# Optimization experiments

Measured on AMD Instinct MI355X. Metric: run time of the kernel, lower is better.

## Reference

```python
import jax, jax.numpy as jnp
import numpy as np

N_HEADS = 6
HEAD_SIZE = 64


def setup_inputs() -> dict:
    key = jax.random.key(0)
    k1, k2, k3, k4 = jax.random.split(key, 4)
    B, T, C = 8, 2048, N_HEADS * HEAD_SIZE
    x = jax.random.normal(k1, (B, T, C), dtype=jnp.float32)
    # small init scale keeps softmax logits in a sane range
    w_qkv = jax.random.normal(k2, (C, 3 * C), dtype=jnp.float32) * 0.05
    w_proj = jax.random.normal(k3, (C, C), dtype=jnp.float32) * 0.05
    b_proj = jax.random.normal(k4, (C,), dtype=jnp.float32) * 0.05
    return {"x": x, "w_qkv": w_qkv, "w_proj": w_proj, "b_proj": b_proj}


def reference(x, w_qkv, w_proj, b_proj):
    B, T, C = x.shape
    qkv = x @ w_qkv                      # [B, T, 3C]
    q, k, v = jnp.split(qkv, 3, axis=2)
    # [B, T, C] -> [B, H, T, D]
    def heads(t):
        return t.reshape(B, T, N_HEADS, HEAD_SIZE).transpose(0, 2, 1, 3)
    q, k, v = heads(q), heads(k), heads(v)
    scale = HEAD_SIZE ** -0.5
    scores = jnp.einsum('bhqd,bhkd->bhqk', q, k) * scale   # [B, H, T, T]
    causal = jnp.tril(jnp.ones((T, T), dtype=bool))
    scores = jnp.where(causal[None, None], scores, jnp.float32(-jnp.inf))
    weights = jax.nn.softmax(scores, axis=-1)
    # dropout is identity in eval mode
    out = jnp.einsum('bhqk,bhkd->bhqd', weights, v)          # [B, H, T, D]
    out = out.transpose(0, 2, 1, 3).reshape(B, T, C)
    return out @ w_proj + b_proj
```

## Files before the change

kernel.cpp:

```cpp
#include <hip/hip_runtime.h>
#include <hip/hip_bf16.h>

typedef __bf16 bf16_t;
typedef __bf16 bf16x8 __attribute__((ext_vector_type(8)));
typedef __bf16 bf16x4 __attribute__((ext_vector_type(4)));
typedef float floatx4 __attribute__((ext_vector_type(4)));
typedef unsigned uint32x2 __attribute__((ext_vector_type(2)));

#define MFMA16(a, b, c) __builtin_amdgcn_mfma_f32_16x16x32_bf16(a, b, c, 0, 0, 0)

#if __has_builtin(__builtin_amdgcn_exp2f)
#define EXP2F(x) __builtin_amdgcn_exp2f(x)
#else
#define EXP2F(x) __expf((x)*0.693147180559945f)
#endif

__device__ __forceinline__ void async_copy16(const bf16_t* g, bf16_t* l) {
    __builtin_amdgcn_global_load_lds((const __attribute__((address_space(1))) void*)g,
                                     (__attribute__((address_space(3))) void*)l, 16, 0, 0);
}

__device__ __forceinline__ unsigned cvt_pk_bf16(float lo, float hi) {
    unsigned r;
    asm("v_cvt_pk_bf16_f32 %0, %1, %2" : "=v"(r) : "v"(lo), "v"(hi));
    return r;
}

__device__ __forceinline__ void plane32(unsigned& x, unsigned& y) {
#if __has_builtin(__builtin_amdgcn_permlane32_swap)
    uint32x2 r = __builtin_amdgcn_permlane32_swap(x, y, false, false);
    x = r[0]; y = r[1];
#else
    asm("v_permlane32_swap_b32 %0, %1" : "+v"(x), "+v"(y));
#endif
}
__device__ __forceinline__ void plane16(unsigned& x, unsigned& y) {
#if __has_builtin(__builtin_amdgcn_permlane16_swap)
    uint32x2 r = __builtin_amdgcn_permlane16_swap(x, y, false, false);
    x = r[0]; y = r[1];
#else
    asm("v_permlane16_swap_b32 %0, %1" : "+v"(x), "+v"(y));
#endif
}

__device__ __forceinline__ bf16x8 pack_pfrag(const floatx4& sE, const floatx4& sO) {
    unsigned a0 = cvt_pk_bf16(sE[0], sE[1]);
    unsigned a1 = cvt_pk_bf16(sE[2], sE[3]);
    unsigned b0 = cvt_pk_bf16(sO[0], sO[1]);
    unsigned b1 = cvt_pk_bf16(sO[2], sO[3]);
    plane32(a0, b0);
    plane32(a1, b1);
    plane16(a0, b0);
    plane16(a1, b1);
    union { unsigned u[4]; bf16x8 v; } r;
    r.u[0] = a0; r.u[1] = a1; r.u[2] = b0; r.u[3] = b1;
    return r.v;
}

__global__ void prep_fused(const float* __restrict__ w_qkv, const float* __restrict__ w_proj,
                           bf16_t* __restrict__ wqkvT, bf16_t* __restrict__ wprojT) {
    const int bx = blockIdx.x, tid = threadIdx.x;
    __shared__ float tile[32][33];
    int which, n0, k0, Nd;
    if (bx < 432) {
        which = 0; Nd = 1152; n0 = (bx % 36) * 32; k0 = (bx / 36) * 32;
    } else {
        int idx = bx - 432;
        which = 1; Nd = 384; n0 = (idx % 12) * 32; k0 = (idx / 12) * 32;
    }
    const float* in = which ? w_proj : w_qkv;
    bf16_t* out = which ? wprojT : wqkvT;
    const int tx = tid & 31, ty = tid >> 5;
#pragma unroll
    for (int i = 0; i < 4; i++)
        tile[ty + i * 8][tx] = in[(size_t)(k0 + ty + i * 8) * Nd + n0 + tx];
    __syncthreads();
#pragma unroll
    for (int i = 0; i < 4; i++) {
        int n = n0 + ty + i * 8;
        float v = tile[tx][ty + i * 8];
        if (!which && n < 384) v *= 0.1803368851f;
        out[(size_t)n * 384 + k0 + tx] = (bf16_t)v;
    }
}

__global__ __launch_bounds__(256, 3)
void gemm_qkv(const float* __restrict__ X, const bf16_t* __restrict__ Bt,
              bf16_t* __restrict__ qkv, bf16_t* __restrict__ Vt, int M, int N, int K) {
    __shared__ __align__(16) bf16_t As[2][128 * 32];
    __shared__ __align__(16) bf16_t Bs[2][128 * 32];
    const int nblk = blockIdx.x;
    const int wgl = ((nblk & 7) * 144) + (nblk >> 3);
    const int row0 = (wgl / 9) * 128, col0 = (wgl % 9) * 128;
    const int tid = threadIdx.x;
    const int wave = tid >> 6, lane = tid & 63;
    const int wm = wave >> 1, wn = wave & 1;
    const int quad = lane >> 4, l16 = lane & 15;
    const int swz = l16 & 3;

    floatx4 acc[4][4];
#pragma unroll
    for (int i = 0; i < 4; i++)
#pragma unroll
        for (int j = 0; j < 4; j++) acc[i][j] = (floatx4){0.f, 0.f, 0.f, 0.f};

    float4 stg[4];
    auto a_load = [&](int k0) {
#pragma unroll
        for (int it = 0; it < 2; it++) {
            int c = wave * 64 + it * 256 + lane;
            int r = c >> 2;
            int col = k0 + (((c & 3) ^ (r & 3)) * 8);
            const float* src = X + (size_t)(row0 + r) * K + col;
            stg[it * 2 + 0] = *(const float4*)src;
            stg[it * 2 + 1] = *(const float4*)(src + 4);
        }
    };
    auto a_write = [&](int buf) {
#pragma unroll
        for (int it = 0; it < 2; it++) {
            float4 v0 = stg[it * 2 + 0], v1 = stg[it * 2 + 1];
            bf16x8 o = {(bf16_t)v0.x, (bf16_t)v0.y, (bf16_t)v0.z, (bf16_t)v0.w,
                        (bf16_t)v1.x, (bf16_t)v1.y, (bf16_t)v1.z, (bf16_t)v1.w};
            *(bf16x8*)(&As[buf][0] + (size_t)(wave * 64 + it * 256 + lane) * 8) = o;
        }
    };
    auto b_stage = [&](int buf, int k0) {
#pragma unroll
        for (int it = 0; it < 2; it++) {
            int cb = wave * 64 + it * 256;
            int c = cb + lane;
            int r = c >> 2;
            int col = k0 + (((c & 3) ^ (r & 3)) * 8);
            async_copy16(Bt + (size_t)(col0 + r) * K + col, &Bs[buf][0] + cb * 8);
        }
    };

    const int nk = K >> 5;
    a_load(0);
    b_stage(0, 0);
    a_write(0);
    for (int kt = 0; kt < nk; kt++) {
        __syncthreads();
        const bool more = (kt + 1 < nk);
        if (more) {
            a_load((kt + 1) * 32);
            b_stage((kt + 1) & 1, (kt + 1) * 32);
        }
        const bf16_t* as = &As[kt & 1][0];
        const bf16_t* bs = &Bs[kt & 1][0];
        bf16x8 af[4], bfr[4];
#pragma unroll
        for (int i = 0; i < 4; i++)
            af[i] = *(const bf16x8*)(as + (wm * 64 + i * 16 + l16) * 32 + ((quad ^ swz) * 8));
#pragma unroll
        for (int j = 0; j < 4; j++)
            bfr[j] = *(const bf16x8*)(bs + (wn * 64 + j * 16 + l16) * 32 + ((quad ^ swz) * 8));
#pragma unroll
        for (int i = 0; i < 4; i++)
#pragma unroll
            for (int j = 0; j < 4; j++) acc[i][j] = MFMA16(bfr[j], af[i], acc[i][j]);
        if (more) a_write((kt + 1) & 1);
    }
    if (col0 < 768) {
#pragma unroll
        for (int i = 0; i < 4; i++) {
            const size_t row = (size_t)(row0 + wm * 64 + i * 16 + l16);
#pragma unroll
            for (int j = 0; j < 4; j++) {
                const int colb = col0 + wn * 64 + j * 16 + quad * 4;
                bf16x4 v = {(bf16_t)acc[i][j][0], (bf16_t)acc[i][j][1],
                            (bf16_t)acc[i][j][2], (bf16_t)acc[i][j][3]};
                *(bf16x4*)(qkv + row * N + colb) = v;
            }
        }
    } else {
        __syncthreads();
        bf16_t* myb = &As[0][0] + wave * 4096;
#pragma unroll
        for (int i = 0; i < 4; i++)
#pragma unroll
            for (int j = 0; j < 4; j++)
#pragma unroll
                for (int r = 0; r < 4; r++) {
                    int d2 = j * 16 + quad * 4 + r;
                    int t2 = i * 16 + l16;
                    myb[d2 * 64 + (((t2 >> 3) ^ (d2 & 7)) * 8) + (t2 & 7)] =
                        (bf16_t)acc[i][j][r];
                }
        asm volatile("s_waitcnt lgkmcnt(0)" ::: "memory");
        const int row_t = row0 + wm * 64;
        const int b = row_t >> 11;
        const int tt = (row_t & 2047) >> 6;
        const int h = (col0 - 768 + wn * 64) >> 6;
        bf16_t* vout = Vt + (((size_t)(b * 6 + h) * 32 + tt) << 12);
#pragma unroll
        for (int it = 0; it < 8; it++) {
            int d2 = it * 8 + (lane >> 3);
            int cl = lane & 7;
            bf16x8 v = *(const bf16x8*)(myb + d2 * 64 + ((cl ^ (d2 & 7)) * 8));
            *(bf16x8*)(vout + d2 * 64 + cl * 8) = v;
        }
    }
}

__global__ __launch_bounds__(256, 3)
void gemm_out(const bf16_t* __restrict__ A, const bf16_t* __restrict__ Bt,
              float* __restrict__ C, int M, int N, int K, const float* __restrict__ bias) {
    __shared__ __align__(16) bf16_t As[2][64 * 32];
    __shared__ __align__(16) bf16_t Bs[2][128 * 32];
    const int nblk = blockIdx.x;
    const int wgl = ((nblk & 7) * 96) + (nblk >> 3);
    const int row0 = (wgl / 3) * 64, col0 = (wgl % 3) * 128;
    const int tid = threadIdx.x;
    const int wave = tid >> 6, lane = tid & 63;
    const int wm = wave >> 1, wn = wave & 1;
    const int quad = lane >> 4, l16 = lane & 15;
    const int swz = l16 & 3;

    floatx4 acc[2][4];
#pragma unroll
    for (int i = 0; i < 2; i++)
#pragma unroll
        for (int j = 0; j < 4; j++) acc[i][j] = (floatx4){0.f, 0.f, 0.f, 0.f};

    auto stage = [&](int buf, int k0) {
        {
            int c = wave * 64 + lane;
            int r = c >> 2;
            int col = k0 + (((c & 3) ^ (r & 3)) * 8);
            async_copy16(A + (size_t)(row0 + r) * K + col, &As[buf][0] + (wave * 64) * 8);
        }
#pragma unroll
        for (int it = 0; it < 2; it++) {
            int cb = wave * 64 + it * 256;
            int c = cb + lane;
            int r = c >> 2;
            int col = k0 + (((c & 3) ^ (r & 3)) * 8);
            async_copy16(Bt + (size_t)(col0 + r) * K + col, &Bs[buf][0] + cb * 8);
        }
    };

    const int nk = K >> 5;
    stage(0, 0);
    for (int kt = 0; kt < nk; kt++) {
        __syncthreads();
        if (kt + 1 < nk) stage((kt + 1) & 1, (kt + 1) * 32);
        const bf16_t* as = &As[kt & 1][0];
        const bf16_t* bs = &Bs[kt & 1][0];
        bf16x8 af[2], bfr[4];
#pragma unroll
        for (int i = 0; i < 2; i++)
            af[i] = *(const bf16x8*)(as + (wm * 32 + i * 16 + l16) * 32 + ((quad ^ swz) * 8));
#pragma unroll
        for (int j = 0; j < 4; j++)
            bfr[j] = *(const bf16x8*)(bs + (wn * 64 + j * 16 + l16) * 32 + ((quad ^ swz) * 8));
#pragma unroll
        for (int i = 0; i < 2; i++)
#pragma unroll
            for (int j = 0; j < 4; j++) acc[i][j] = MFMA16(bfr[j], af[i], acc[i][j]);
    }
#pragma unroll
    for (int i = 0; i < 2; i++) {
        const size_t row = (size_t)(row0 + wm * 32 + i * 16 + l16);
#pragma unroll
        for (int j = 0; j < 4; j++) {
            const int colb = col0 + wn * 64 + j * 16 + quad * 4;
            float4 bv = *(const float4*)(bias + colb);
            float4 v = {acc[i][j][0] + bv.x, acc[i][j][1] + bv.y,
                        acc[i][j][2] + bv.z, acc[i][j][3] + bv.w};
            *(float4*)(C + row * N + colb) = v;
        }
    }
}

__device__ __forceinline__ void stage64(const bf16_t* __restrict__ gtile, int stride,
                                        bf16_t* lds, int wave, int lane) {
#pragma unroll
    for (int it = 0; it < 2; it++) {
        int cb = wave * 64 + it * 256;
        int c = cb + lane;
        int r = c >> 3;
        int col = ((c & 7) ^ (r & 7)) * 8;
        async_copy16(gtile + (size_t)r * stride + col, lds + cb * 8);
    }
}

__global__ __launch_bounds__(256, 3)
void attn_kernel(const bf16_t* __restrict__ qkv, const bf16_t* __restrict__ Vt,
                 bf16_t* __restrict__ attn_out) {
    constexpr int T = 2048, C3 = 1152;
    const int nblk = blockIdx.x;
    const int wgl = ((nblk & 7) * 96) + (nblk >> 3);
    const int bx = wgl & 15;
    const int g = wgl >> 4;
    const int h = g % 6, b = g / 6;
    const int qa = bx, qb = 31 - bx;
    const int tid = threadIdx.x;
    const int wave = tid >> 6, lane = tid & 63;
    const int quad = lane >> 4, l16 = lane & 15;

    __shared__ __align__(16) bf16_t Ks[2][64 * 64];
    __shared__ __align__(16) bf16_t Vs[2][64 * 64];

    const bf16_t* kbase = qkv + (size_t)b * T * C3 + 384 + h * 64;
    const bf16_t* vbase = Vt + (((size_t)(b * 6 + h) * 32) << 12);

    const bf16_t* qpa =
        qkv + ((size_t)b * T + qa * 64 + wave * 16 + l16) * C3 + h * 64 + quad * 8;
    const bf16_t* qpb =
        qkv + ((size_t)b * T + qb * 64 + wave * 16 + l16) * C3 + h * 64 + quad * 8;
    bf16x8 qA0 = *(const bf16x8*)qpa, qA1 = *(const bf16x8*)(qpa + 32);
    bf16x8 qB0 = *(const bf16x8*)qpb, qB1 = *(const bf16x8*)(qpb + 32);

    floatx4 oA[4], oB[4];
    float lpA = 0.f, lpB = 0.f;
#pragma unroll
    for (int r = 0; r < 4; r++) {
        oA[r] = (floatx4){0.f, 0.f, 0.f, 0.f};
        oB[r] = (floatx4){0.f, 0.f, 0.f, 0.f};
    }
    const floatx4 C0 = {-13.f, -13.f, -13.f, -13.f};

    stage64(kbase, C3, &Ks[0][0], wave, lane);
    stage64(vbase, 64, &Vs[0][0], wave, lane);

    const int swz = l16 & 7;

    for (int kt = 0; kt <= qb; kt++) {
        __syncthreads();
        if (kt < qb) {
            stage64(kbase + (size_t)(kt + 1) * 64 * C3, C3, &Ks[(kt + 1) & 1][0], wave, lane);
            stage64(vbase + ((kt + 1) << 12), 64, &Vs[(kt + 1) & 1][0], wave, lane);
        }
        const bf16_t* kb = &Ks[kt & 1][0];
        const bf16_t* vb = &Vs[kt & 1][0];
        const bool doA = (kt <= qa);

        bf16x8 kf[4][2];
#pragma unroll
        for (int nt = 0; nt < 4; nt++)
#pragma unroll
            for (int hh = 0; hh < 2; hh++)
                kf[nt][hh] = *(const bf16x8*)(kb + (nt * 16 + l16) * 64 +
                                              (((hh * 4 + quad) ^ swz) * 8));

        floatx4 sA[4], sB[4];
        __builtin_amdgcn_s_setprio(1);
#pragma unroll
        for (int nt = 0; nt < 4; nt++) {
            sB[nt] = MFMA16(kf[nt][0], qB0, C0);
            sB[nt] = MFMA16(kf[nt][1], qB1, sB[nt]);
        }
        if (doA) {
#pragma unroll
            for (int nt = 0; nt < 4; nt++) {
                sA[nt] = MFMA16(kf[nt][0], qA0, C0);
                sA[nt] = MFMA16(kf[nt][1], qA1, sA[nt]);
            }
        }
        __builtin_amdgcn_s_setprio(0);

        bf16x8 vf[4][2];
#pragma unroll
        for (int nt = 0; nt < 4; nt++)
#pragma unroll
            for (int hh = 0; hh < 2; hh++)
                vf[nt][hh] = *(const bf16x8*)(vb + (nt * 16 + l16) * 64 +
                                              (((hh * 4 + quad) ^ swz) * 8));

        if (kt == qb) {
#pragma unroll
            for (int nt = 0; nt < 4; nt++)
#pragma unroll
                for (int r = 0; r < 4; r++)
                    if (nt * 16 + quad * 4 + r > wave * 16 + l16) sB[nt][r] = -1e30f;
        }
        if (kt == qa) {
#pragma unroll
            for (int nt = 0; nt < 4; nt++)
#pragma unroll
                for (int r = 0; r < 4; r++)
                    if (nt * 16 + quad * 4 + r > wave * 16 + l16) sA[nt][r] = -1e30f;
        }

#pragma unroll
        for (int nt = 0; nt < 4; nt++)
#pragma unroll
            for (int r = 0; r < 4; r++) {
                float p = EXP2F(sB[nt][r]);
                sB[nt][r] = p;
                lpB += p;
            }
        bf16x8 pB0 = pack_pfrag(sB[0], sB[1]);
        bf16x8 pB1 = pack_pfrag(sB[2], sB[3]);

        bf16x8 pA0, pA1;
        if (doA) {
#pragma unroll
            for (int nt = 0; nt < 4; nt++)
#pragma unroll
                for (int r = 0; r < 4; r++) {
                    float p = EXP2F(sA[nt][r]);
                    sA[nt][r] = p;
                    lpA += p;
                }
            pA0 = pack_pfrag(sA[0], sA[1]);
            pA1 = pack_pfrag(sA[2], sA[3]);
        }

        __builtin_amdgcn_s_setprio(1);
#pragma unroll
        for (int dt = 0; dt < 4; dt++) {
            oB[dt] = MFMA16(vf[dt][0], pB0, oB[dt]);
            oB[dt] = MFMA16(vf[dt][1], pB1, oB[dt]);
        }
        if (doA) {
#pragma unroll
            for (int dt = 0; dt < 4; dt++) {
                oA[dt] = MFMA16(vf[dt][0], pA0, oA[dt]);
                oA[dt] = MFMA16(vf[dt][1], pA1, oA[dt]);
            }
        }
        __builtin_amdgcn_s_setprio(0);
    }

    lpA += __shfl_xor(lpA, 16); lpA += __shfl_xor(lpA, 32);
    lpB += __shfl_xor(lpB, 16); lpB += __shfl_xor(lpB, 32);
    const float invA = 1.0f / lpA, invB = 1.0f / lpB;
    const int tA = qa * 64 + wave * 16 + l16, tB = qb * 64 + wave * 16 + l16;
#pragma unroll
    for (int dt = 0; dt < 4; dt++) {
        bf16x4 va = {(bf16_t)(oA[dt][0] * invA), (bf16_t)(oA[dt][1] * invA),
                     (bf16_t)(oA[dt][2] * invA), (bf16_t)(oA[dt][3] * invA)};
        bf16x4 vb4 = {(bf16_t)(oB[dt][0] * invB), (bf16_t)(oB[dt][1] * invB),
                      (bf16_t)(oB[dt][2] * invB), (bf16_t)(oB[dt][3] * invB)};
        int col = h * 64 + dt * 16 + quad * 4;
        *(bf16x4*)(attn_out + ((size_t)b * T + tA) * 384 + col) = va;
        *(bf16x4*)(attn_out + ((size_t)b * T + tB) * 384 + col) = vb4;
    }
}

extern "C" void kernel_launch(void* const* d_in, const int* in_sizes, int n_in,
                              void* d_out, int out_size, void* d_ws, size_t ws_size,
                              hipStream_t stream) {
    const float* x      = (const float*)d_in[0];
    const float* w_qkv  = (const float*)d_in[1];
    const float* w_proj = (const float*)d_in[2];
    const float* b_proj = (const float*)d_in[3];
    float* out = (float*)d_out;

    bf16_t* ws = (bf16_t*)d_ws;
    bf16_t* wqkvT = ws;
    bf16_t* wprojT = wqkvT + 1152 * 384;
    bf16_t* qkv = wprojT + 384 * 384;
    bf16_t* Vt = qkv + (size_t)16384 * 1152;
    bf16_t* attn = Vt + (size_t)48 * 64 * 2048;

    hipLaunchKernelGGL(prep_fused, dim3(432 + 144), dim3(256), 0, stream,
                       w_qkv, w_proj, wqkvT, wprojT);
    hipLaunchKernelGGL(gemm_qkv, dim3(1152), dim3(256), 0, stream,
                       x, wqkvT, qkv, Vt, 16384, 1152, 384);
    hipLaunchKernelGGL(attn_kernel, dim3(768), dim3(256), 0, stream, qkv, Vt, attn);
    hipLaunchKernelGGL(gemm_out, dim3(768), dim3(256), 0, stream,
                       attn, wprojT, out, 16384, 384, 384, b_proj);
}
```

Baseline: 163.6 us.

## Load V tiles straight from global into registers, bypassing LDS staging

V tiles (pre-transposed in Vt) are now read from global memory directly into registers at the top of each key-tile iteration instead of being double-buffered through shared memory. The K fragment loads are also interleaved with the score MFMAs per sub-tile rather than loaded all up front. This halves LDS usage and LDS traffic, which may raise occupancy, but exposes global-load latency for V within the iteration and adds register pressure.

```diff
diff --git a/kernel.cpp b/kernel.cpp
--- a/kernel.cpp
+++ b/kernel.cpp
@@ -301,7 +301,6 @@
     const int quad = lane >> 4, l16 = lane & 15;
 
     __shared__ __align__(16) bf16_t Ks[2][64 * 64];
-    __shared__ __align__(16) bf16_t Vs[2][64 * 64];
 
     const bf16_t* kbase = qkv + (size_t)b * T * C3 + 384 + h * 64;
     const bf16_t* vbase = Vt + (((size_t)(b * 6 + h) * 32) << 12);
@@ -323,51 +322,38 @@
     const floatx4 C0 = {-13.f, -13.f, -13.f, -13.f};
 
     stage64(kbase, C3, &Ks[0][0], wave, lane);
-    stage64(vbase, 64, &Vs[0][0], wave, lane);
 
     const int swz = l16 & 7;
 
     for (int kt = 0; kt <= qb; kt++) {
         __syncthreads();
-        if (kt < qb) {
+        bf16x8 vf[4][2];
+        const bf16_t* vt = vbase + ((size_t)kt << 12);
+#pragma unroll
+        for (int nt = 0; nt < 4; nt++)
+#pragma unroll
+            for (int hh = 0; hh < 2; hh++)
+                vf[nt][hh] = *(const bf16x8*)(vt + (nt * 16 + l16) * 64 +
+                                              (hh * 4 + quad) * 8);
+        if (kt < qb)
             stage64(kbase + (size_t)(kt + 1) * 64 * C3, C3, &Ks[(kt + 1) & 1][0], wave, lane);
-            stage64(vbase + ((kt + 1) << 12), 64, &Vs[(kt + 1) & 1][0], wave, lane);
-        }
         const bf16_t* kb = &Ks[kt & 1][0];
-        const bf16_t* vb = &Vs[kt & 1][0];
         const bool doA = (kt <= qa);
-
-        bf16x8 kf[4][2];
-#pragma unroll
-        for (int nt = 0; nt < 4; nt++)
-#pragma unroll
-            for (int hh = 0; hh < 2; hh++)
-                kf[nt][hh] = *(const bf16x8*)(kb + (nt * 16 + l16) * 64 +
-                                              (((hh * 4 + quad) ^ swz) * 8));
 
         floatx4 sA[4], sB[4];
         __builtin_amdgcn_s_setprio(1);
 #pragma unroll
         for (int nt = 0; nt < 4; nt++) {
-            sB[nt] = MFMA16(kf[nt][0], qB0, C0);
-            sB[nt] = MFMA16(kf[nt][1], qB1, sB[nt]);
-        }
-        if (doA) {
-#pragma unroll
-            for (int nt = 0; nt < 4; nt++) {
-                sA[nt] = MFMA16(kf[nt][0], qA0, C0);
-                sA[nt] = MFMA16(kf[nt][1], qA1, sA[nt]);
+            bf16x8 kf0 = *(const bf16x8*)(kb + (nt * 16 + l16) * 64 + ((quad ^ swz) * 8));
+            bf16x8 kf1 = *(const bf16x8*)(kb + (nt * 16 + l16) * 64 + (((4 + quad) ^ swz) * 8));
+            sB[nt] = MFMA16(kf0, qB0, C0);
+            sB[nt] = MFMA16(kf1, qB1, sB[nt]);
+            if (doA) {
+                sA[nt] = MFMA16(kf0, qA0, C0);
+                sA[nt] = MFMA16(kf1, qA1, sA[nt]);
             }
         }
         __builtin_amdgcn_s_setprio(0);
-
-        bf16x8 vf[4][2];
-#pragma unroll
-        for (int nt = 0; nt < 4; nt++)
-#pragma unroll
-            for (int hh = 0; hh < 2; hh++)
-                vf[nt][hh] = *(const bf16x8*)(vb + (nt * 16 + l16) * 64 +
-                                              (((hh * 4 + quad) ^ swz) * 8));
 
         if (kt == qb) {
 #pragma unroll
```

Result: slower. 226.1 us (+38.2%).
